# Kernel tuning notes

Hardware: AMD Instinct MI355X
Metric: run time of the kernel (lower is better)

The kernel has to match this reference:

```python
import jax, jax.numpy as jnp
import numpy as np

N = 50000      # num nodes
E = 600000     # num edges (avg degree 12)
IN = 256       # in_feats
H = 128        # h_feats
P = 2          # prop_step
LN_EPS = 1e-5


def setup_inputs() -> dict:
    key = jax.random.key(0)
    ks = jax.random.split(key, 8)
    return {
        "in_feat": jax.random.normal(ks[0], (N, IN), jnp.float32),
        "row": jax.random.randint(ks[1], (E,), 0, N),  # target node of each edge
        "col": jax.random.randint(ks[2], (E,), 0, N),  # source node of each edge
        "lin_w": jax.random.normal(ks[3], (H, IN), jnp.float32) / np.sqrt(IN).astype(np.float32),
        "lin_b": jnp.zeros((H,), jnp.float32),
        "conv_w": jax.random.normal(ks[4], (H, H), jnp.float32) / np.sqrt(H).astype(np.float32),
        "conv_b": jnp.zeros((H,), jnp.float32),
        "root_emb": jax.random.normal(ks[5], (1, H), jnp.float32) * 0.02,
        "ln_gamma": jnp.ones((P, H), jnp.float32),
        "ln_beta": jnp.zeros((P, H), jnp.float32),
    }


def _layernorm(x, g, b):
    mu = jnp.mean(x, axis=-1, keepdims=True)
    var = jnp.mean(jnp.square(x - mu), axis=-1, keepdims=True)
    return (x - mu) * jax.lax.rsqrt(var + LN_EPS) * g + b


def reference(in_feat, row, col, lin_w, lin_b, conv_w, conv_b, root_emb, ln_gamma, ln_beta):
    n = in_feat.shape[0]
    h = in_feat @ lin_w.T + lin_b                      # [N, H]

    # OGB-style degree norm with +1 trick (original edges, row = target)
    deg = jax.ops.segment_sum(jnp.ones_like(row, dtype=h.dtype), row, num_segments=n) + 1.0
    deg_inv = 1.0 / deg                                # deg >= 1, never inf

    # GCNConv symmetric norm with self loops: D^-1/2 (A+I) D^-1/2
    loop = jnp.arange(n)
    r2 = jnp.concatenate([row, loop])                  # [E+N] targets
    c2 = jnp.concatenate([col, loop])                  # [E+N] sources
    d2 = jax.ops.segment_sum(jnp.ones_like(r2, dtype=h.dtype), r2, num_segments=n)
    dis = jnp.where(d2 > 0, jax.lax.rsqrt(jnp.maximum(d2, 1.0)), 0.0)
    ew = dis[r2] * dis[c2]                             # [E+N] edge weights

    root = root_emb[0]                                 # [H]
    ori = h
    for i in range(P):
        if i != 0:
            h = h + ori                                # residual
            h = _layernorm(h, ln_gamma[i], ln_beta[i])
            h = jax.nn.relu(h)
            # dropout=0.0 -> identity
        xw = h @ conv_w.T                              # [N, H]
        h_msg = jax.ops.segment_sum(ew[:, None] * xw[c2], r2, num_segments=n) + conv_b
        root_contrib = jax.nn.relu(h + root) * deg_inv[:, None]
        h = h_msg + root_contrib
    return h
```

## Files before the change

### kernel.cpp

```cpp
#include <hip/hip_runtime.h>

#define NN 50000
#define EE 600000
#define INF 256
#define HF 128
#define CEB ((EE + 255) / 256)

typedef __attribute__((ext_vector_type(8))) short short8;
typedef __attribute__((ext_vector_type(4))) float floatx4;

__device__ __forceinline__ unsigned short f32_to_bf16_rne(float x) {
    unsigned int u = __float_as_uint(x);
    unsigned int r = (u + 0x7FFFu + ((u >> 16) & 1u)) >> 16;
    return (unsigned short)r;
}
__device__ __forceinline__ float bf16_to_f32(unsigned short h) {
    return __uint_as_float(((unsigned int)h) << 16);
}
__device__ __forceinline__ float bf16lo_u32(unsigned int u) {
    return __uint_as_float(u << 16);
}
__device__ __forceinline__ float bf16hi_u32(unsigned int u) {
    return __uint_as_float(u & 0xFFFF0000u);
}
__device__ __forceinline__ void cvt_hilo8(float4 v0, float4 v1, short8& hs, short8& ls) {
    float x[8] = {v0.x, v0.y, v0.z, v0.w, v1.x, v1.y, v1.z, v1.w};
    union { short8 s; unsigned short u[8]; } H, L;
#pragma unroll
    for (int k = 0; k < 8; ++k) {
        unsigned short hi = f32_to_bf16_rne(x[k]);
        H.u[k] = hi;
        L.u[k] = f32_to_bf16_rne(x[k] - bf16_to_f32(hi));
    }
    hs = H.s;
    ls = L.s;
}

__global__ void count_and_prepack(const int* __restrict__ row, int* __restrict__ cnt,
                                  int* __restrict__ pos, int E,
                                  const float* __restrict__ lw, const float* __restrict__ cw,
                                  unsigned short* __restrict__ fl, unsigned short* __restrict__ fc) {
    int b = blockIdx.x;
    if (b < CEB) {
        int e = b * 256 + threadIdx.x;
        if (e < E) pos[e] = atomicAdd(&cnt[row[e]], 1);
        return;
    }
    int idx = (b - CEB) * 256 + threadIdx.x;
    const float* src;
    unsigned short* dst;
    int K, c;
    if (idx < 8192) {
        src = lw; dst = fl; K = INF; c = idx;
    } else if (idx < 12288) {
        src = cw; dst = fc; K = HF; c = idx - 8192;
    } else return;
    int lane = c & 63;
    int nt = (c >> 6) & 7;
    int hl = (c >> 9) & 1;
    int kc = c >> 10;
    int rw = nt * 16 + (lane & 15);
    int koff = kc * 32 + (lane >> 4) * 8;
    const float* p = &src[(size_t)rw * K + koff];
    float4 v0 = *reinterpret_cast<const float4*>(p);
    float4 v1 = *reinterpret_cast<const float4*>(p + 4);
    short8 hs, ls;
    cvt_hilo8(v0, v1, hs, ls);
    *reinterpret_cast<short8*>(&dst[(size_t)c * 8]) = hl ? ls : hs;
}

__global__ void scan_phase1(const int* __restrict__ cnt, int* __restrict__ bsum, int n) {
    __shared__ int sdata[256];
    int t = threadIdx.x;
    int i = blockIdx.x * 256 + t;
    sdata[t] = (i < n) ? cnt[i] : 0;
    __syncthreads();
    for (int s = 128; s > 0; s >>= 1) {
        if (t < s) sdata[t] += sdata[t + s];
        __syncthreads();
    }
    if (t == 0) bsum[blockIdx.x] = sdata[0];
}

__global__ void scan_phase3(const int* __restrict__ cnt, const int* __restrict__ bsum,
                            int* __restrict__ row_start,
                            float* __restrict__ deg_inv, float* __restrict__ dis,
                            int n, int nb, int E) {
    __shared__ int sb[256];
    __shared__ int sdata[256];
    int t = threadIdx.x;
    sb[t] = (t < nb) ? bsum[t] : 0;
    __syncthreads();
    for (int s = 1; s < 256; s <<= 1) {
        int add = (t >= s) ? sb[t - s] : 0;
        __syncthreads();
        sb[t] += add;
        __syncthreads();
    }
    int base = sb[blockIdx.x] - bsum[blockIdx.x];
    int i = blockIdx.x * 256 + t;
    int v = (i < n) ? cnt[i] : 0;
    sdata[t] = v;
    __syncthreads();
    for (int s = 1; s < 256; s <<= 1) {
        int add = (t >= s) ? sdata[t - s] : 0;
        __syncthreads();
        sdata[t] += add;
        __syncthreads();
    }
    if (i < n) {
        int ex = base + sdata[t] - v;
        row_start[i] = ex;
        float d = (float)(v + 1);
        deg_inv[i] = 1.0f / d;
        dis[i] = rsqrtf(d);
    }
    if (blockIdx.x == 0 && t == 0) row_start[n] = E;
}

__global__ void fill_csr(const int* __restrict__ row, const int* __restrict__ col,
                         const int* __restrict__ row_start, const int* __restrict__ pos,
                         int* __restrict__ csr_col, int E) {
    int e = blockIdx.x * blockDim.x + threadIdx.x;
    if (e < E) {
        int p = row_start[row[e]] + pos[e];
        __builtin_nontemporal_store(col[e], &csr_col[p]);
    }
}

template <int K, int MODE>
__global__ __launch_bounds__(256) void gemm_ldsw(
    const float* __restrict__ Af,
    const unsigned short* __restrict__ Ahg, const unsigned short* __restrict__ Alg,
    const unsigned short* __restrict__ Wf,
    const float* __restrict__ bias,
    float* __restrict__ C, unsigned short* __restrict__ Cbf,
    const float* __restrict__ h, const float* __restrict__ deg_inv,
    const float* __restrict__ dis, const float* __restrict__ root,
    const float* __restrict__ gamma, const float* __restrict__ beta,
    int M) {
    constexpr int NKC = K / 32;
    __shared__ unsigned short WS[2 * 8192];

    const int t = threadIdx.x;
    const int wave = t >> 6;
    const int lane = t & 63;
    const int lrow = lane & 15;
    const int quad = lane >> 4;
    const int bm = blockIdx.x * 64;
    int arow = bm + wave * 16 + lrow;
    if (arow >= M) arow = M - 1;

    floatx4 acc[8];
#pragma unroll
    for (int nt = 0; nt < 8; ++nt) acc[nt] = (floatx4){0.f, 0.f, 0.f, 0.f};

#pragma unroll
    for (int p = 0; p < NKC / 2; ++p) {
        if (p) __syncthreads();
        {
            const uint4* src = reinterpret_cast<const uint4*>(Wf + (size_t)p * 16384);
            uint4* dstl = reinterpret_cast<uint4*>(WS);
#pragma unroll
            for (int i = 0; i < 8; ++i) dstl[t + 256 * i] = src[t + 256 * i];
        }
        __syncthreads();
#pragma unroll
        for (int k2 = 0; k2 < 2; ++k2) {
            int kc = p * 2 + k2;
            short8 afh, afl;
            if (MODE == 0) {
                const float* ap = &Af[(size_t)arow * K + kc * 32 + quad * 8];
                float4 a0 = *reinterpret_cast<const float4*>(ap);
                float4 a1 = *reinterpret_cast<const float4*>(ap + 4);
                cvt_hilo8(a0, a1, afh, afl);
            } else {
                size_t ao = (size_t)arow * K + kc * 32 + quad * 8;
                afh = *reinterpret_cast<const short8*>(&Ahg[ao]);
                afl = *reinterpret_cast<const short8*>(&Alg[ao]);
            }
            const unsigned short* wb = &WS[k2 * 8192 + lane * 8];
#pragma unroll
            for (int nt = 0; nt < 8; ++nt) {
                short8 bfh = *reinterpret_cast<const short8*>(wb + nt * 512);
                short8 bfl = *reinterpret_cast<const short8*>(wb + 4096 + nt * 512);
                acc[nt] = __builtin_amdgcn_mfma_f32_16x16x32_bf16(afh, bfh, acc[nt], 0, 0, 0);
                acc[nt] = __builtin_amdgcn_mfma_f32_16x16x32_bf16(afl, bfh, acc[nt], 0, 0, 0);
                acc[nt] = __builtin_amdgcn_mfma_f32_16x16x32_bf16(afh, bfl, acc[nt], 0, 0, 0);
            }
        }
    }

    float cb[8], rt[8], gm[8], bt[8];
#pragma unroll
    for (int nt = 0; nt < 8; ++nt) {
        int colh = nt * 16 + lrow;
        cb[nt] = bias[colh];
        if (MODE >= 1) rt[nt] = root[colh];
        if (MODE == 1) { gm[nt] = gamma[colh]; bt[nt] = beta[colh]; }
    }

#pragma unroll
    for (int r = 0; r < 4; ++r) {
        int grow = bm + wave * 16 + quad * 4 + r;
        bool ok = (grow < M);
        int gr = ok ? grow : M - 1;
        float x[8];
        if (MODE == 0) {
#pragma unroll
            for (int nt = 0; nt < 8; ++nt) x[nt] = acc[nt][r] + cb[nt];
        } else {
            float di = deg_inv[gr];
            float hv[8];
#pragma unroll
            for (int nt = 0; nt < 8; ++nt) hv[nt] = h[(size_t)gr * HF + nt * 16 + lrow];
#pragma unroll
            for (int nt = 0; nt < 8; ++nt) {
                float v = acc[nt][r] + cb[nt] + fmaxf(hv[nt] + rt[nt], 0.f) * di;
                x[nt] = (MODE == 1) ? v + hv[nt] : v;
            }
        }
        if (MODE == 1) {
            float s = 0.f;
#pragma unroll
            for (int nt = 0; nt < 8; ++nt) s += x[nt];
#pragma unroll
            for (int m = 1; m < 16; m <<= 1) s += __shfl_xor(s, m, 64);
            float mu = s * (1.0f / HF);
            float var = 0.f;
#pragma unroll
            for (int nt = 0; nt < 8; ++nt) { float d = x[nt] - mu; var += d * d; }
#pragma unroll
            for (int m = 1; m < 16; m <<= 1) var += __shfl_xor(var, m, 64);
            float rs = rsqrtf(var * (1.0f / HF) + 1e-5f);
            float ds = dis[gr];
            if (ok) {
#pragma unroll
                for (int nt = 0; nt < 8; ++nt) {
                    int colh = nt * 16 + lrow;
                    float y = fmaxf((x[nt] - mu) * rs * gm[nt] + bt[nt], 0.f);
                    C[(size_t)grow * HF + colh] = y;
                    Cbf[(size_t)grow * HF + colh] = f32_to_bf16_rne(ds * y);
                }
            }
        } else if (MODE == 0) {
            if (ok) {
                float ds = dis[grow];
#pragma unroll
                for (int nt = 0; nt < 8; ++nt) {
                    int colh = nt * 16 + lrow;
                    C[(size_t)grow * HF + colh] = x[nt];
                    Cbf[(size_t)grow * HF + colh] = f32_to_bf16_rne(ds * x[nt]);
                }
            }
        } else {
            if (ok) {
#pragma unroll
                for (int nt = 0; nt < 8; ++nt)
                    C[(size_t)grow * HF + nt * 16 + lrow] = x[nt];
            }
        }
    }
}

__global__ void aggregate(const int* __restrict__ row_start, const int* __restrict__ csr_col,
                          const float* __restrict__ dis, const float* __restrict__ deg_inv,
                          const float* __restrict__ h, const unsigned short* __restrict__ hbf,
                          unsigned short* __restrict__ agg_hi, unsigned short* __restrict__ agg_lo,
                          int n) {
    int wid = (blockIdx.x * blockDim.x + threadIdx.x) >> 6;
    int lane = threadIdx.x & 63;
    if (wid >= n) return;
    int q = lane >> 4;
    int l16 = lane & 15;
    int s = row_start[wid];
    int e = row_start[wid + 1];
    float a0 = 0.f, a1 = 0.f, a2 = 0.f, a3 = 0.f, a4 = 0.f, a5 = 0.f, a6 = 0.f, a7 = 0.f;
    if (e - s <= 16) {
        int j0 = s + q;
        bool p0 = j0 < e, p1 = j0 + 4 < e, p2 = j0 + 8 < e, p3 = j0 + 12 < e;
        int c0 = p0 ? csr_col[j0] : 0;
        int c1 = p1 ? csr_col[j0 + 4] : 0;
        int c2 = p2 ? csr_col[j0 + 8] : 0;
        int c3 = p3 ? csr_col[j0 + 12] : 0;
        uint4 z = make_uint4(0, 0, 0, 0);
        uint4 g0 = z, g1 = z, g2 = z, g3 = z;
        if (p0) g0 = *reinterpret_cast<const uint4*>(&hbf[(size_t)c0 * HF + l16 * 8]);
        if (p1) g1 = *reinterpret_cast<const uint4*>(&hbf[(size_t)c1 * HF + l16 * 8]);
        if (p2) g2 = *reinterpret_cast<const uint4*>(&hbf[(size_t)c2 * HF + l16 * 8]);
        if (p3) g3 = *reinterpret_cast<const uint4*>(&hbf[(size_t)c3 * HF + l16 * 8]);
        a0 = bf16lo_u32(g0.x) + bf16lo_u32(g1.x) + bf16lo_u32(g2.x) + bf16lo_u32(g3.x);
        a1 = bf16hi_u32(g0.x) + bf16hi_u32(g1.x) + bf16hi_u32(g2.x) + bf16hi_u32(g3.x);
        a2 = bf16lo_u32(g0.y) + bf16lo_u32(g1.y) + bf16lo_u32(g2.y) + bf16lo_u32(g3.y);
        a3 = bf16hi_u32(g0.y) + bf16hi_u32(g1.y) + bf16hi_u32(g2.y) + bf16hi_u32(g3.y);
        a4 = bf16lo_u32(g0.z) + bf16lo_u32(g1.z) + bf16lo_u32(g2.z) + bf16lo_u32(g3.z);
        a5 = bf16hi_u32(g0.z) + bf16hi_u32(g1.z) + bf16hi_u32(g2.z) + bf16hi_u32(g3.z);
        a6 = bf16lo_u32(g0.w) + bf16lo_u32(g1.w) + bf16lo_u32(g2.w) + bf16lo_u32(g3.w);
        a7 = bf16hi_u32(g0.w) + bf16hi_u32(g1.w) + bf16hi_u32(g2.w) + bf16hi_u32(g3.w);
    } else {
        float b0 = 0.f, b1 = 0.f, b2 = 0.f, b3 = 0.f, b4 = 0.f, b5 = 0.f, b6 = 0.f, b7 = 0.f;
        int j = s + q;
        for (; j + 4 < e; j += 8) {
            int c0 = csr_col[j];
            int c1 = csr_col[j + 4];
            uint4 h0 = *reinterpret_cast<const uint4*>(&hbf[(size_t)c0 * HF + l16 * 8]);
            uint4 h1 = *reinterpret_cast<const uint4*>(&hbf[(size_t)c1 * HF + l16 * 8]);
            a0 += bf16lo_u32(h0.x); a1 += bf16hi_u32(h0.x);
            a2 += bf16lo_u32(h0.y); a3 += bf16hi_u32(h0.y);
            a4 += bf16lo_u32(h0.z); a5 += bf16hi_u32(h0.z);
            a6 += bf16lo_u32(h0.w); a7 += bf16hi_u32(h0.w);
            b0 += bf16lo_u32(h1.x); b1 += bf16hi_u32(h1.x);
            b2 += bf16lo_u32(h1.y); b3 += bf16hi_u32(h1.y);
            b4 += bf16lo_u32(h1.z); b5 += bf16hi_u32(h1.z);
            b6 += bf16lo_u32(h1.w); b7 += bf16hi_u32(h1.w);
        }
        if (j < e) {
            int c0 = csr_col[j];
            uint4 h0 = *reinterpret_cast<const uint4*>(&hbf[(size_t)c0 * HF + l16 * 8]);
            a0 += bf16lo_u32(h0.x); a1 += bf16hi_u32(h0.x);
            a2 += bf16lo_u32(h0.y); a3 += bf16hi_u32(h0.y);
            a4 += bf16lo_u32(h0.z); a5 += bf16hi_u32(h0.z);
            a6 += bf16lo_u32(h0.w); a7 += bf16hi_u32(h0.w);
        }
        a0 += b0; a1 += b1; a2 += b2; a3 += b3;
        a4 += b4; a5 += b5; a6 += b6; a7 += b7;
    }
#pragma unroll
    for (int m = 16; m < 64; m <<= 1) {
        a0 += __shfl_xor(a0, m, 64);
        a1 += __shfl_xor(a1, m, 64);
        a2 += __shfl_xor(a2, m, 64);
        a3 += __shfl_xor(a3, m, 64);
        a4 += __shfl_xor(a4, m, 64);
        a5 += __shfl_xor(a5, m, 64);
        a6 += __shfl_xor(a6, m, 64);
        a7 += __shfl_xor(a7, m, 64);
    }
    if (q == 0) {
        float dn = dis[wid];
        float di = deg_inv[wid];
        float4 hA = *reinterpret_cast<const float4*>(&h[(size_t)wid * HF + l16 * 8]);
        float4 hB = *reinterpret_cast<const float4*>(&h[(size_t)wid * HF + l16 * 8 + 4]);
        float o[8];
        o[0] = fmaf(dn, a0, di * hA.x);
        o[1] = fmaf(dn, a1, di * hA.y);
        o[2] = fmaf(dn, a2, di * hA.z);
        o[3] = fmaf(dn, a3, di * hA.w);
        o[4] = fmaf(dn, a4, di * hB.x);
        o[5] = fmaf(dn, a5, di * hB.y);
        o[6] = fmaf(dn, a6, di * hB.z);
        o[7] = fmaf(dn, a7, di * hB.w);
        unsigned short hi[8], lo[8];
#pragma unroll
        for (int k = 0; k < 8; ++k) {
            hi[k] = f32_to_bf16_rne(o[k]);
            lo[k] = f32_to_bf16_rne(o[k] - bf16_to_f32(hi[k]));
        }
        uint4 hp, lp;
        hp.x = (unsigned)hi[0] | ((unsigned)hi[1] << 16);
        hp.y = (unsigned)hi[2] | ((unsigned)hi[3] << 16);
        hp.z = (unsigned)hi[4] | ((unsigned)hi[5] << 16);
        hp.w = (unsigned)hi[6] | ((unsigned)hi[7] << 16);
        lp.x = (unsigned)lo[0] | ((unsigned)lo[1] << 16);
        lp.y = (unsigned)lo[2] | ((unsigned)lo[3] << 16);
        lp.z = (unsigned)lo[4] | ((unsigned)lo[5] << 16);
        lp.w = (unsigned)lo[6] | ((unsigned)lo[7] << 16);
        *reinterpret_cast<uint4*>(&agg_hi[(size_t)wid * HF + l16 * 8]) = hp;
        *reinterpret_cast<uint4*>(&agg_lo[(size_t)wid * HF + l16 * 8]) = lp;
    }
}

extern "C" void kernel_launch(void* const* d_in, const int* in_sizes, int n_in,
                              void* d_out, int out_size, void* d_ws, size_t ws_size,
                              hipStream_t stream) {
    const int N = NN, E = EE;
    const float* in_feat = (const float*)d_in[0];
    const int* row = (const int*)d_in[1];
    const int* col = (const int*)d_in[2];
    const float* lin_w = (const float*)d_in[3];
    const float* lin_b = (const float*)d_in[4];
    const float* conv_w = (const float*)d_in[5];
    const float* conv_b = (const float*)d_in[6];
    const float* root_emb = (const float*)d_in[7];
    const float* ln_gamma = (const float*)d_in[8];
    const float* ln_beta = (const float*)d_in[9];
    float* out = (float*)d_out;

    float* ws = (float*)d_ws;
    size_t o = 0;
    float* deg_inv = ws + o; o += N;
    float* dis = ws + o; o += N;
    int* cnt = (int*)(ws + o); o += N;
    int* row_start = (int*)(ws + o); o += N + 4;
    int* pos = (int*)(ws + o); o += E;
    int* bsum = (int*)(ws + o); o += 256;
    int* csr_col = (int*)(ws + o); o += E;
    o = (o + 3) & ~(size_t)3;
    unsigned short* fl = (unsigned short*)(ws + o); o += 32768;
    unsigned short* fc = (unsigned short*)(ws + o); o += 16384;
    float* h0 = ws + o; o += (size_t)N * HF;
    unsigned short* hbf = (unsigned short*)(ws + o); o += (size_t)N * HF / 2;
    unsigned short* agg_hi = (unsigned short*)(ws + o); o += (size_t)N * HF / 2;
    unsigned short* agg_lo = (unsigned short*)(ws + o); o += (size_t)N * HF / 2;

    const int NB = (N + 255) / 256;

    hipMemsetAsync(cnt, 0, N * sizeof(int), stream);
    count_and_prepack<<<CEB + 48, 256, 0, stream>>>(row, cnt, pos, E, lin_w, conv_w, fl, fc);
    scan_phase1<<<NB, 256, 0, stream>>>(cnt, bsum, N);
    scan_phase3<<<NB, 256, 0, stream>>>(cnt, bsum, row_start, deg_inv, dis, N, NB, E);
    fill_csr<<<CEB, 256, 0, stream>>>(row, col, row_start, pos, csr_col, E);

    const int GB = (N + 63) / 64;
    const int WB = (N + 3) / 4;

    gemm_ldsw<INF, 0><<<GB, 256, 0, stream>>>(in_feat, nullptr, nullptr, fl, lin_b,
                                              h0, hbf, nullptr, nullptr, dis, nullptr,
                                              nullptr, nullptr, N);

    aggregate<<<WB, 256, 0, stream>>>(row_start, csr_col, dis, deg_inv, h0, hbf,
                                      agg_hi, agg_lo, N);
    gemm_ldsw<HF, 1><<<GB, 256, 0, stream>>>(nullptr, agg_hi, agg_lo, fc, conv_b,
                                             h0, hbf, h0, deg_inv, dis, root_emb,
                                             ln_gamma + HF, ln_beta + HF, N);

    aggregate<<<WB, 256, 0, stream>>>(row_start, csr_col, dis, deg_inv, h0, hbf,
                                      agg_hi, agg_lo, N);
    gemm_ldsw<HF, 2><<<GB, 256, 0, stream>>>(nullptr, agg_hi, agg_lo, fc, conv_b,
                                             out, nullptr, h0, deg_inv, dis, root_emb,
                                             nullptr, nullptr, N);
}
```

Baseline: 290.3 us.

## Fuse neighbor aggregation into conv GEMM prologue and CSR fill into first GEMM

Each conv GEMM block now gathers and sums the neighbor bf16 rows for its own 64 nodes, then applies the dis/deg_inv combination. It splits the result into hi/lo bf16 fragments in registers, so the separate aggregate kernel and its agg_hi/agg_lo round trip through global memory go away. The CSR fill work runs as extra leading blocks of the first GEMM launch, which removes another launch. The bf16 feature buffer is double-buffered so a conv pass never overwrites rows that other blocks are still gathering. The cost is that each thread now walks its node's neighbor list serially, with degree-divergent loops and fewer waves devoted to gathering, which may hide latency less well than the old wave-per-node kernel.

Result: no change. 292.3 us (+0.7%).

```diff
diff --git a/kernel.cpp b/kernel.cpp
--- a/kernel.cpp
+++ b/kernel.cpp
@@ -118,38 +118,113 @@
     if (blockIdx.x == 0 && t == 0) row_start[n] = E;
 }
 
-__global__ void fill_csr(const int* __restrict__ row, const int* __restrict__ col,
-                         const int* __restrict__ row_start, const int* __restrict__ pos,
-                         int* __restrict__ csr_col, int E) {
-    int e = blockIdx.x * blockDim.x + threadIdx.x;
-    if (e < E) {
-        int p = row_start[row[e]] + pos[e];
-        __builtin_nontemporal_store(col[e], &csr_col[p]);
-    }
-}
-
 template <int K, int MODE>
-__global__ __launch_bounds__(256) void gemm_ldsw(
+__global__ __launch_bounds__(256) void gemm_fused(
     const float* __restrict__ Af,
-    const unsigned short* __restrict__ Ahg, const unsigned short* __restrict__ Alg,
+    const unsigned short* __restrict__ hbf_in,
     const unsigned short* __restrict__ Wf,
     const float* __restrict__ bias,
     float* __restrict__ C, unsigned short* __restrict__ Cbf,
     const float* __restrict__ h, const float* __restrict__ deg_inv,
     const float* __restrict__ dis, const float* __restrict__ root,
     const float* __restrict__ gamma, const float* __restrict__ beta,
-    int M) {
+    const int* __restrict__ row_start, int* __restrict__ csr_col,
+    const int* __restrict__ row, const int* __restrict__ col,
+    const int* __restrict__ pos, int fill_blocks, int M) {
     constexpr int NKC = K / 32;
     __shared__ unsigned short WS[2 * 8192];
+
+    int bidx = blockIdx.x;
+    if (MODE == 0) {
+        if (bidx < fill_blocks) {
+            int e = bidx * 256 + threadIdx.x;
+            if (e < EE) {
+                int pp = row_start[row[e]] + pos[e];
+                __builtin_nontemporal_store(col[e], &csr_col[pp]);
+            }
+            return;
+        }
+        bidx -= fill_blocks;
+    }
 
     const int t = threadIdx.x;
     const int wave = t >> 6;
     const int lane = t & 63;
     const int lrow = lane & 15;
     const int quad = lane >> 4;
-    const int bm = blockIdx.x * 64;
+    const int bm = bidx * 64;
     int arow = bm + wave * 16 + lrow;
     if (arow >= M) arow = M - 1;
+
+    short8 ah[NKC], al[NKC];
+    if (MODE >= 1) {
+        const int node = arow;
+        int s = row_start[node];
+        int e = row_start[node + 1];
+        float a[NKC][8];
+#pragma unroll
+        for (int kc = 0; kc < NKC; ++kc)
+#pragma unroll
+            for (int k = 0; k < 8; ++k) a[kc][k] = 0.f;
+        int j = s;
+        for (; j + 1 < e; j += 2) {
+            int c0 = csr_col[j];
+            int c1 = csr_col[j + 1];
+            const unsigned short* p0 = &hbf_in[(size_t)c0 * HF + quad * 8];
+            const unsigned short* p1 = &hbf_in[(size_t)c1 * HF + quad * 8];
+            uint4 g0[NKC], g1[NKC];
+#pragma unroll
+            for (int kc = 0; kc < NKC; ++kc) {
+                g0[kc] = *reinterpret_cast<const uint4*>(p0 + kc * 32);
+                g1[kc] = *reinterpret_cast<const uint4*>(p1 + kc * 32);
+            }
+#pragma unroll
+            for (int kc = 0; kc < NKC; ++kc) {
+                a[kc][0] += bf16lo_u32(g0[kc].x) + bf16lo_u32(g1[kc].x);
+                a[kc][1] += bf16hi_u32(g0[kc].x) + bf16hi_u32(g1[kc].x);
+                a[kc][2] += bf16lo_u32(g0[kc].y) + bf16lo_u32(g1[kc].y);
+                a[kc][3] += bf16hi_u32(g0[kc].y) + bf16hi_u32(g1[kc].y);
+                a[kc][4] += bf16lo_u32(g0[kc].z) + bf16lo_u32(g1[kc].z);
+                a[kc][5] += bf16hi_u32(g0[kc].z) + bf16hi_u32(g1[kc].z);
+                a[kc][6] += bf16lo_u32(g0[kc].w) + bf16lo_u32(g1[kc].w);
+                a[kc][7] += bf16hi_u32(g0[kc].w) + bf16hi_u32(g1[kc].w);
+            }
+        }
+        if (j < e) {
+            int c0 = csr_col[j];
+            const unsigned short* p0 = &hbf_in[(size_t)c0 * HF + quad * 8];
+#pragma unroll
+            for (int kc = 0; kc < NKC; ++kc) {
+                uint4 g = *reinterpret_cast<const uint4*>(p0 + kc * 32);
+                a[kc][0] += bf16lo_u32(g.x);
+                a[kc][1] += bf16hi_u32(g.x);
+                a[kc][2] += bf16lo_u32(g.y);
+                a[kc][3] += bf16hi_u32(g.y);
+                a[kc][4] += bf16lo_u32(g.z);
+                a[kc][5] += bf16hi_u32(g.z);
+                a[kc][6] += bf16lo_u32(g.w);
+                a[kc][7] += bf16hi_u32(g.w);
+            }
+        }
+        float dn = dis[node];
+        float di = deg_inv[node];
+#pragma unroll
+        for (int kc = 0; kc < NKC; ++kc) {
+            const float* hp = &h[(size_t)node * HF + kc * 32 + quad * 8];
+            float4 hv0 = *reinterpret_cast<const float4*>(hp);
+            float4 hv1 = *reinterpret_cast<const float4*>(hp + 4);
+            float4 o0, o1;
+            o0.x = fmaf(dn, a[kc][0], di * hv0.x);
+            o0.y = fmaf(dn, a[kc][1], di * hv0.y);
+            o0.z = fmaf(dn, a[kc][2], di * hv0.z);
+            o0.w = fmaf(dn, a[kc][3], di * hv0.w);
+            o1.x = fmaf(dn, a[kc][4], di * hv1.x);
+            o1.y = fmaf(dn, a[kc][5], di * hv1.y);
+            o1.z = fmaf(dn, a[kc][6], di * hv1.z);
+            o1.w = fmaf(dn, a[kc][7], di * hv1.w);
+            cvt_hilo8(o0, o1, ah[kc], al[kc]);
+        }
+    }
 
     floatx4 acc[8];
 #pragma unroll
@@ -175,9 +250,8 @@
                 float4 a1 = *reinterpret_cast<const float4*>(ap + 4);
                 cvt_hilo8(a0, a1, afh, afl);
             } else {
-                size_t ao = (size_t)arow * K + kc * 32 + quad * 8;
-                afh = *reinterpret_cast<const short8*>(&Ahg[ao]);
-                afl = *reinterpret_cast<const short8*>(&Alg[ao]);
+                afh = ah[kc];
+                afl = al[kc];
             }
             const unsigned short* wb = &WS[k2 * 8192 + lane * 8];
 #pragma unroll
@@ -260,113 +334,6 @@
                     C[(size_t)grow * HF + nt * 16 + lrow] = x[nt];
             }
         }
-    }
-}
-
-__global__ void aggregate(const int* __restrict__ row_start, const int* __restrict__ csr_col,
-                          const float* __restrict__ dis, const float* __restrict__ deg_inv,
-                          const float* __restrict__ h, const unsigned short* __restrict__ hbf,
-                          unsigned short* __restrict__ agg_hi, unsigned short* __restrict__ agg_lo,
-                          int n) {
-    int wid = (blockIdx.x * blockDim.x + threadIdx.x) >> 6;
-    int lane = threadIdx.x & 63;
-    if (wid >= n) return;
-    int q = lane >> 4;
-    int l16 = lane & 15;
-    int s = row_start[wid];
-    int e = row_start[wid + 1];
-    float a0 = 0.f, a1 = 0.f, a2 = 0.f, a3 = 0.f, a4 = 0.f, a5 = 0.f, a6 = 0.f, a7 = 0.f;
-    if (e - s <= 16) {
-        int j0 = s + q;
-        bool p0 = j0 < e, p1 = j0 + 4 < e, p2 = j0 + 8 < e, p3 = j0 + 12 < e;
-        int c0 = p0 ? csr_col[j0] : 0;
-        int c1 = p1 ? csr_col[j0 + 4] : 0;
-        int c2 = p2 ? csr_col[j0 + 8] : 0;
-        int c3 = p3 ? csr_col[j0 + 12] : 0;
-        uint4 z = make_uint4(0, 0, 0, 0);
-        uint4 g0 = z, g1 = z, g2 = z, g3 = z;
-        if (p0) g0 = *reinterpret_cast<const uint4*>(&hbf[(size_t)c0 * HF + l16 * 8]);
-        if (p1) g1 = *reinterpret_cast<const uint4*>(&hbf[(size_t)c1 * HF + l16 * 8]);
-        if (p2) g2 = *reinterpret_cast<const uint4*>(&hbf[(size_t)c2 * HF + l16 * 8]);
-        if (p3) g3 = *reinterpret_cast<const uint4*>(&hbf[(size_t)c3 * HF + l16 * 8]);
-        a0 = bf16lo_u32(g0.x) + bf16lo_u32(g1.x) + bf16lo_u32(g2.x) + bf16lo_u32(g3.x);
-        a1 = bf16hi_u32(g0.x) + bf16hi_u32(g1.x) + bf16hi_u32(g2.x) + bf16hi_u32(g3.x);
-        a2 = bf16lo_u32(g0.y) + bf16lo_u32(g1.y) + bf16lo_u32(g2.y) + bf16lo_u32(g3.y);
-        a3 = bf16hi_u32(g0.y) + bf16hi_u32(g1.y) + bf16hi_u32(g2.y) + bf16hi_u32(g3.y);
-        a4 = bf16lo_u32(g0.z) + bf16lo_u32(g1.z) + bf16lo_u32(g2.z) + bf16lo_u32(g3.z);
-        a5 = bf16hi_u32(g0.z) + bf16hi_u32(g1.z) + bf16hi_u32(g2.z) + bf16hi_u32(g3.z);
-        a6 = bf16lo_u32(g0.w) + bf16lo_u32(g1.w) + bf16lo_u32(g2.w) + bf16lo_u32(g3.w);
-        a7 = bf16hi_u32(g0.w) + bf16hi_u32(g1.w) + bf16hi_u32(g2.w) + bf16hi_u32(g3.w);
-    } else {
-        float b0 = 0.f, b1 = 0.f, b2 = 0.f, b3 = 0.f, b4 = 0.f, b5 = 0.f, b6 = 0.f, b7 = 0.f;
-        int j = s + q;
-        for (; j + 4 < e; j += 8) {
-            int c0 = csr_col[j];
-            int c1 = csr_col[j + 4];
-            uint4 h0 = *reinterpret_cast<const uint4*>(&hbf[(size_t)c0 * HF + l16 * 8]);
-            uint4 h1 = *reinterpret_cast<const uint4*>(&hbf[(size_t)c1 * HF + l16 * 8]);
-            a0 += bf16lo_u32(h0.x); a1 += bf16hi_u32(h0.x);
-            a2 += bf16lo_u32(h0.y); a3 += bf16hi_u32(h0.y);
-            a4 += bf16lo_u32(h0.z); a5 += bf16hi_u32(h0.z);
-            a6 += bf16lo_u32(h0.w); a7 += bf16hi_u32(h0.w);
-            b0 += bf16lo_u32(h1.x); b1 += bf16hi_u32(h1.x);
-            b2 += bf16lo_u32(h1.y); b3 += bf16hi_u32(h1.y);
-            b4 += bf16lo_u32(h1.z); b5 += bf16hi_u32(h1.z);
-            b6 += bf16lo_u32(h1.w); b7 += bf16hi_u32(h1.w);
-        }
-        if (j < e) {
-            int c0 = csr_col[j];
-            uint4 h0 = *reinterpret_cast<const uint4*>(&hbf[(size_t)c0 * HF + l16 * 8]);
-            a0 += bf16lo_u32(h0.x); a1 += bf16hi_u32(h0.x);
-            a2 += bf16lo_u32(h0.y); a3 += bf16hi_u32(h0.y);
-            a4 += bf16lo_u32(h0.z); a5 += bf16hi_u32(h0.z);
-            a6 += bf16lo_u32(h0.w); a7 += bf16hi_u32(h0.w);
-        }
-        a0 += b0; a1 += b1; a2 += b2; a3 += b3;
-        a4 += b4; a5 += b5; a6 += b6; a7 += b7;
-    }
-#pragma unroll
-    for (int m = 16; m < 64; m <<= 1) {
-        a0 += __shfl_xor(a0, m, 64);
-        a1 += __shfl_xor(a1, m, 64);
-        a2 += __shfl_xor(a2, m, 64);
-        a3 += __shfl_xor(a3, m, 64);
-        a4 += __shfl_xor(a4, m, 64);
-        a5 += __shfl_xor(a5, m, 64);
-        a6 += __shfl_xor(a6, m, 64);
-        a7 += __shfl_xor(a7, m, 64);
-    }
-    if (q == 0) {
-        float dn = dis[wid];
-        float di = deg_inv[wid];
-        float4 hA = *reinterpret_cast<const float4*>(&h[(size_t)wid * HF + l16 * 8]);
-        float4 hB = *reinterpret_cast<const float4*>(&h[(size_t)wid * HF + l16 * 8 + 4]);
-        float o[8];
-        o[0] = fmaf(dn, a0, di * hA.x);
-        o[1] = fmaf(dn, a1, di * hA.y);
-        o[2] = fmaf(dn, a2, di * hA.z);
-        o[3] = fmaf(dn, a3, di * hA.w);
-        o[4] = fmaf(dn, a4, di * hB.x);
-        o[5] = fmaf(dn, a5, di * hB.y);
-        o[6] = fmaf(dn, a6, di * hB.z);
-        o[7] = fmaf(dn, a7, di * hB.w);
-        unsigned short hi[8], lo[8];
-#pragma unroll
-        for (int k = 0; k < 8; ++k) {
-            hi[k] = f32_to_bf16_rne(o[k]);
-            lo[k] = f32_to_bf16_rne(o[k] - bf16_to_f32(hi[k]));
-        }
-        uint4 hp, lp;
-        hp.x = (unsigned)hi[0] | ((unsigned)hi[1] << 16);
-        hp.y = (unsigned)hi[2] | ((unsigned)hi[3] << 16);
-        hp.z = (unsigned)hi[4] | ((unsigned)hi[5] << 16);
-        hp.w = (unsigned)hi[6] | ((unsigned)hi[7] << 16);
-        lp.x = (unsigned)lo[0] | ((unsigned)lo[1] << 16);
-        lp.y = (unsigned)lo[2] | ((unsigned)lo[3] << 16);
-        lp.z = (unsigned)lo[4] | ((unsigned)lo[5] << 16);
-        lp.w = (unsigned)lo[6] | ((unsigned)lo[7] << 16);
-        *reinterpret_cast<uint4*>(&agg_hi[(size_t)wid * HF + l16 * 8]) = hp;
-        *reinterpret_cast<uint4*>(&agg_lo[(size_t)wid * HF + l16 * 8]) = lp;
     }
 }
 
@@ -400,33 +367,28 @@
     unsigned short* fc = (unsigned short*)(ws + o); o += 16384;
     float* h0 = ws + o; o += (size_t)N * HF;
     unsigned short* hbf = (unsigned short*)(ws + o); o += (size_t)N * HF / 2;
-    unsigned short* agg_hi = (unsigned short*)(ws + o); o += (size_t)N * HF / 2;
-    unsigned short* agg_lo = (unsigned short*)(ws + o); o += (size_t)N * HF / 2;
+    unsigned short* hbf2 = (unsigned short*)(ws + o); o += (size_t)N * HF / 2;
 
     const int NB = (N + 255) / 256;
+    const int GB = (N + 63) / 64;
 
     hipMemsetAsync(cnt, 0, N * sizeof(int), stream);
     count_and_prepack<<<CEB + 48, 256, 0, stream>>>(row, cnt, pos, E, lin_w, conv_w, fl, fc);
     scan_phase1<<<NB, 256, 0, stream>>>(cnt, bsum, N);
     scan_phase3<<<NB, 256, 0, stream>>>(cnt, bsum, row_start, deg_inv, dis, N, NB, E);
-    fill_csr<<<CEB, 256, 0, stream>>>(row, col, row_start, pos, csr_col, E);
-
-    const int GB = (N + 63) / 64;
-    const int WB = (N + 3) / 4;
-
-    gemm_ldsw<INF, 0><<<GB, 256, 0, stream>>>(in_feat, nullptr, nullptr, fl, lin_b,
-                                              h0, hbf, nullptr, nullptr, dis, nullptr,
-                                              nullptr, nullptr, N);
-
-    aggregate<<<WB, 256, 0, stream>>>(row_start, csr_col, dis, deg_inv, h0, hbf,
-                                      agg_hi, agg_lo, N);
-    gemm_ldsw<HF, 1><<<GB, 256, 0, stream>>>(nullptr, agg_hi, agg_lo, fc, conv_b,
-                                             h0, hbf, h0, deg_inv, dis, root_emb,
-                                             ln_gamma + HF, ln_beta + HF, N);
-
-    aggregate<<<WB, 256, 0, stream>>>(row_start, csr_col, dis, deg_inv, h0, hbf,
-                                      agg_hi, agg_lo, N);
-    gemm_ldsw<HF, 2><<<GB, 256, 0, stream>>>(nullptr, agg_hi, agg_lo, fc, conv_b,
-                                             out, nullptr, h0, deg_inv, dis, root_emb,
-                                             nullptr, nullptr, N);
-}
+
+    gemm_fused<INF, 0><<<CEB + GB, 256, 0, stream>>>(
+        in_feat, nullptr, fl, lin_b, h0, hbf,
+        nullptr, nullptr, dis, nullptr, nullptr, nullptr,
+        row_start, csr_col, row, col, pos, CEB, N);
+
+    gemm_fused<HF, 1><<<GB, 256, 0, stream>>>(
+        nullptr, hbf, fc, conv_b, h0, hbf2,
+        h0, deg_inv, dis, root_emb, ln_gamma + HF, ln_beta + HF,
+        row_start, csr_col, nullptr, nullptr, nullptr, 0, N);
+
+    gemm_fused<HF, 2><<<GB, 256, 0, stream>>>(
+        nullptr, hbf2, fc, conv_b, out, nullptr,
+        h0, deg_inv, dis, root_emb, nullptr, nullptr,
+        row_start, csr_col, nullptr, nullptr, nullptr, 0, N);
+}
```
